# Optimization experiments

Hardware: AMD Instinct MI355X
Metric: run time of the kernel (lower is better)

## Reference

```python
import jax, jax.numpy as jnp
import numpy as np

B, T, C = 2, 4096, 768
NH = 12
HD = C // NH  # 64


def setup_inputs() -> dict:
    key = jax.random.key(0)
    k0, k1, k2, k3, k4 = jax.random.split(key, 5)
    x = jax.random.normal(k0, (B, T, C), dtype=jnp.float32)
    # parameters (stored as [in, out] for x @ W)
    w_attn = jax.random.normal(k1, (C, 3 * C), dtype=jnp.float32) * 0.02
    b_attn = jnp.zeros((3 * C,), dtype=jnp.float32)
    w_proj = jax.random.normal(k2, (C, C), dtype=jnp.float32) * 0.02
    b_proj = jnp.zeros((C,), dtype=jnp.float32)
    return {"x": x, "w_attn": w_attn, "b_attn": b_attn, "w_proj": w_proj, "b_proj": b_proj}


def reference(x, w_attn, b_attn, w_proj, b_proj):
    Bv, Tv, Cv = x.shape
    qkv = x @ w_attn + b_attn  # (B,T,3C)
    q, k, v = jnp.split(qkv, 3, axis=2)
    # (B, NH, T, HD)
    q = q.reshape(Bv, Tv, NH, HD).transpose(0, 2, 1, 3)
    k = k.reshape(Bv, Tv, NH, HD).transpose(0, 2, 1, 3)
    v = v.reshape(Bv, Tv, NH, HD).transpose(0, 2, 1, 3)
    att = jnp.einsum('bhqd,bhkd->bhqk', q, k) / jnp.sqrt(jnp.float32(HD))
    causal = jnp.tril(jnp.ones((Tv, Tv), dtype=bool))  # mask buffer slice
    att = jnp.where(causal[None, None, :, :], att, jnp.float32(-jnp.inf))
    att = jax.nn.softmax(att, axis=-1)
    y = jnp.einsum('bhqk,bhkd->bhqd', att, v)
    y = y.transpose(0, 2, 1, 3).reshape(Bv, Tv, Cv)
    y = y @ w_proj + b_proj
    return y
```

## Files before the change

### kernel.cpp

```cpp
#include <hip/hip_runtime.h>

typedef __bf16 bf16;
typedef float f32x4 __attribute__((ext_vector_type(4)));
typedef bf16 bf16x8v __attribute__((ext_vector_type(8)));
typedef bf16 bf16x4v __attribute__((ext_vector_type(4)));

#define MFMA_BF16(a, b, c) __builtin_amdgcn_mfma_f32_16x16x32_bf16((a), (b), (c), 0, 0, 0)

__device__ __forceinline__ void async16(const bf16* g, bf16* l) {
  __builtin_amdgcn_global_load_lds(
      (const __attribute__((address_space(1))) void*)g,
      (__attribute__((address_space(3))) void*)l, 16, 0, 0);
}

__global__ __launch_bounds__(256) void convert_kernel(
    const float* __restrict__ in, bf16* __restrict__ out, int n8) {
  int i = blockIdx.x * 256 + threadIdx.x;
  if (i >= n8) return;
  const float4* p = (const float4*)in + (size_t)i * 2;
  float4 a = p[0], b = p[1];
  bf16x8v o;
  o[0] = (bf16)a.x; o[1] = (bf16)a.y; o[2] = (bf16)a.z; o[3] = (bf16)a.w;
  o[4] = (bf16)b.x; o[5] = (bf16)b.y; o[6] = (bf16)b.z; o[7] = (bf16)b.w;
  ((bf16x8v*)out)[i] = o;
}

__global__ __launch_bounds__(256) void transpose_conv_kernel(
    const float* __restrict__ in, bf16* __restrict__ out, int R, int Ccols) {
  __shared__ float tile[32][33];
  int c0 = blockIdx.x * 32, r0 = blockIdx.y * 32;
  int tx = threadIdx.x & 31;
  int ty = threadIdx.x >> 5;
#pragma unroll
  for (int i = 0; i < 4; ++i) {
    int r = ty + i * 8;
    tile[r][tx] = in[(size_t)(r0 + r) * Ccols + c0 + tx];
  }
  __syncthreads();
#pragma unroll
  for (int i = 0; i < 4; ++i) {
    int c = ty + i * 8;
    out[(size_t)(c0 + c) * R + r0 + tx] = (bf16)tile[tx][c];
  }
}

__global__ __launch_bounds__(256) void transpose_bf16_kernel(
    const bf16* __restrict__ in, bf16* __restrict__ out, int R, int Ccols) {
  __shared__ bf16 tile[32][33];
  const bf16* inp = in + (size_t)blockIdx.z * R * Ccols;
  bf16* outp = out + (size_t)blockIdx.z * R * Ccols;
  int c0 = blockIdx.x * 32, r0 = blockIdx.y * 32;
  int tx = threadIdx.x & 31;
  int ty = threadIdx.x >> 5;
#pragma unroll
  for (int i = 0; i < 4; ++i) {
    int r = ty + i * 8;
    tile[r][tx] = inp[(size_t)(r0 + r) * Ccols + c0 + tx];
  }
  __syncthreads();
#pragma unroll
  for (int i = 0; i < 4; ++i) {
    int c = ty + i * 8;
    outp[(size_t)(c0 + c) * R + r0 + tx] = tile[tx][c];
  }
}

template <int MODE>
__global__ __launch_bounds__(256) void gemm_kernel(
    const bf16* __restrict__ A, const bf16* __restrict__ Bt,
    const float* __restrict__ bias, int N, float* __restrict__ outf,
    bf16* __restrict__ qo, bf16* __restrict__ ko, bf16* __restrict__ vo) {
  constexpr int Kdim = 768;
  __shared__ __align__(16) bf16 As[128][32];
  __shared__ __align__(16) bf16 Bs[128][32];
  const int tid = threadIdx.x;
  const int lane = tid & 63;
  const int wave = tid >> 6;
  const int wm = (wave >> 1) * 64, wn = (wave & 1) * 64;
  const int m0 = blockIdx.y * 128, n0 = blockIdx.x * 128;
  const int l15 = lane & 15, q4 = lane >> 4;

  f32x4 acc[4][4] = {};

  const int ca = wave * 2;
  const int ar = lane >> 2;
  const int ac = (lane & 3) * 8;
  bf16* asBase = &As[0][0];
  bf16* bsBase = &Bs[0][0];

  for (int k0 = 0; k0 < Kdim; k0 += 32) {
    const bf16* gA = A + (size_t)(m0 + ca * 16 + ar) * Kdim + k0 + ac;
    async16(gA, asBase + ca * 512);
    async16(gA + 16 * Kdim, asBase + (ca + 1) * 512);
    const bf16* gB = Bt + (size_t)(n0 + ca * 16 + ar) * Kdim + k0 + ac;
    async16(gB, bsBase + ca * 512);
    async16(gB + 16 * Kdim, bsBase + (ca + 1) * 512);
    __syncthreads();
    bf16x8v af[4], bfg[4];
#pragma unroll
    for (int i = 0; i < 4; ++i)
      af[i] = *(const bf16x8v*)&As[wm + i * 16 + l15][q4 * 8];
#pragma unroll
    for (int i = 0; i < 4; ++i)
      bfg[i] = *(const bf16x8v*)&Bs[wn + i * 16 + l15][q4 * 8];
#pragma unroll
    for (int mi = 0; mi < 4; ++mi)
#pragma unroll
      for (int ni = 0; ni < 4; ++ni)
        acc[mi][ni] = MFMA_BF16(af[mi], bfg[ni], acc[mi][ni]);
    __syncthreads();
  }

#pragma unroll
  for (int mi = 0; mi < 4; ++mi) {
#pragma unroll
    for (int ni = 0; ni < 4; ++ni) {
      int col = n0 + wn + ni * 16 + l15;
      float bv = bias[col];
#pragma unroll
      for (int r = 0; r < 4; ++r) {
        int row = m0 + wm + mi * 16 + q4 * 4 + r;
        float val = acc[mi][ni][r] + bv;
        if (MODE == 0) {
          outf[(size_t)row * N + col] = val;
        } else {
          int sel = col / 768;
          int cc = col - sel * 768;
          int h = cc >> 6, d = cc & 63;
          int b = row >> 12, t = row & 4095;
          bf16* dst = sel == 0 ? qo : (sel == 1 ? ko : vo);
          dst[((size_t)(b * 12 + h) * 4096 + t) * 64 + d] = (bf16)val;
        }
      }
    }
  }
}

__global__ __launch_bounds__(256, 3) void attn_kernel(
    const bf16* __restrict__ q, const bf16* __restrict__ k,
    const bf16* __restrict__ vt, bf16* __restrict__ y) {
  __shared__ __align__(16) bf16 Kb[2][64][64];
  __shared__ __align__(16) bf16 Vb[2][64][64];
  __shared__ __align__(16) bf16 Ps[4][32][64];
  const int tid = threadIdx.x;
  const int lane = tid & 63, wave = tid >> 6;
  const int l15 = lane & 15, q4 = lane >> 4;
  const int swz = l15 & 7;
  const int id = blockIdx.x;
  const int bh = id % 24;
  const int p = id / 24;
  const int rs0 = (63 - p) * 64 + wave * 16;
  const int rs1 = p * 64 + wave * 16;
  const int hb = bh % 12, bb = bh / 12;

  const int gr = lane >> 3;
  const int sj = (lane & 7) ^ gr;
  const bf16* kgbase = k + (size_t)bh * 4096 * 64;
  const bf16* vgbase = vt + (size_t)bh * 64 * 4096;

  bf16x8v ones;
#pragma unroll
  for (int j = 0; j < 8; ++j) ones[j] = (bf16)1.0f;

  bf16x8v qf[2][2];
#pragma unroll
  for (int st = 0; st < 2; ++st) {
    const int rs = st ? rs1 : rs0;
    const bf16* qrow = q + ((size_t)bh * 4096 + rs + l15) * 64 + q4 * 8;
#pragma unroll
    for (int ks = 0; ks < 2; ++ks) {
      bf16x8v t8 = *(const bf16x8v*)(qrow + ks * 32);
#pragma unroll
      for (int j = 0; j < 8; ++j) t8[j] = (bf16)((float)t8[j] * 0.18033688f);
      qf[st][ks] = t8;
    }
  }

  f32x4 o0[4] = {}, o1[4] = {};
  f32x4 ol0 = {}, ol1 = {};

  auto stage = [&](int kt, int buf) {
    const int t0k = kt * 64;
#pragma unroll
    for (int g = 0; g < 2; ++g) {
      const int grp = wave * 2 + g;
      async16(kgbase + (size_t)(t0k + grp * 8 + gr) * 64 + sj * 8,
              &Kb[buf][grp * 8][0]);
      async16(vgbase + (size_t)(grp * 8 + gr) * 4096 + t0k + sj * 8,
              &Vb[buf][grp * 8][0]);
    }
  };

  auto sm_full = [&](f32x4 (&s)[4]) {
#pragma unroll
    for (int ni = 0; ni < 4; ++ni)
#pragma unroll
      for (int r = 0; r < 4; ++r)
        s[ni][r] = __builtin_amdgcn_exp2f(s[ni][r] - 28.8539008f);
  };
  auto sm_mask = [&](f32x4 (&s)[4], int lim) {
#pragma unroll
    for (int ni = 0; ni < 4; ++ni)
#pragma unroll
      for (int r = 0; r < 4; ++r)
        s[ni][r] = (ni * 16 + q4 * 4 + r <= lim)
                       ? __builtin_amdgcn_exp2f(s[ni][r] - 28.8539008f)
                       : 0.0f;
  };
  auto pwrite = [&](const f32x4 (&s)[4], int row) {
#pragma unroll
    for (int ni = 0; ni < 4; ++ni) {
      bf16x4v pv4;
#pragma unroll
      for (int e = 0; e < 4; ++e) pv4[e] = (bf16)s[ni][e];
      const int jb = ni * 2 + (q4 >> 1);
      *(bf16x4v*)&Ps[wave][row][((jb ^ (row & 7)) * 8) + (q4 & 1) * 4] = pv4;
    }
  };

  const int ktmax = 64 - p;
  stage(0, 0);

  for (int kt = 0; kt < ktmax; ++kt) {
    const int buf = kt & 1;
    __syncthreads();
    if (kt + 1 < ktmax) stage(kt + 1, buf ^ 1);
    const int t0 = kt * 64;
    const bool act1 = (t0 <= rs1 + 15);

    f32x4 s0[4] = {}, s1[4] = {};
    __builtin_amdgcn_s_setprio(1);
    if (act1) {
#pragma unroll
      for (int ni = 0; ni < 4; ++ni) {
#pragma unroll
        for (int ks = 0; ks < 2; ++ks) {
          bf16x8v kf = *(const bf16x8v*)&Kb[buf][ni * 16 + l15]
                                           [((ks * 4 + q4) ^ swz) * 8];
          s0[ni] = MFMA_BF16(kf, qf[0][ks], s0[ni]);
          s1[ni] = MFMA_BF16(kf, qf[1][ks], s1[ni]);
        }
      }
    } else {
#pragma unroll
      for (int ni = 0; ni < 4; ++ni) {
#pragma unroll
        for (int ks = 0; ks < 2; ++ks) {
          bf16x8v kf = *(const bf16x8v*)&Kb[buf][ni * 16 + l15]
                                           [((ks * 4 + q4) ^ swz) * 8];
          s0[ni] = MFMA_BF16(kf, qf[0][ks], s0[ni]);
        }
      }
    }
    __builtin_amdgcn_s_setprio(0);

    if (t0 + 63 <= rs0) sm_full(s0); else sm_mask(s0, rs0 + l15 - t0);
    pwrite(s0, l15);
    if (act1) {
      if (t0 + 63 <= rs1) sm_full(s1); else sm_mask(s1, rs1 + l15 - t0);
      pwrite(s1, 16 + l15);
    }

    bf16x8v pf0[2], pf1[2];
#pragma unroll
    for (int ks = 0; ks < 2; ++ks)
      pf0[ks] = *(const bf16x8v*)&Ps[wave][l15][((ks * 4 + q4) ^ swz) * 8];
    if (act1) {
#pragma unroll
      for (int ks = 0; ks < 2; ++ks)
        pf1[ks] =
            *(const bf16x8v*)&Ps[wave][16 + l15][((ks * 4 + q4) ^ swz) * 8];
      __builtin_amdgcn_s_setprio(1);
#pragma unroll
      for (int d4 = 0; d4 < 4; ++d4) {
#pragma unroll
        for (int ks = 0; ks < 2; ++ks) {
          bf16x8v vf = *(const bf16x8v*)&Vb[buf][d4 * 16 + l15]
                                           [((ks * 4 + q4) ^ swz) * 8];
          o0[d4] = MFMA_BF16(pf0[ks], vf, o0[d4]);
          o1[d4] = MFMA_BF16(pf1[ks], vf, o1[d4]);
        }
      }
#pragma unroll
      for (int ks = 0; ks < 2; ++ks) {
        ol0 = MFMA_BF16(pf0[ks], ones, ol0);
        ol1 = MFMA_BF16(pf1[ks], ones, ol1);
      }
      __builtin_amdgcn_s_setprio(0);
    } else {
      __builtin_amdgcn_s_setprio(1);
#pragma unroll
      for (int d4 = 0; d4 < 4; ++d4) {
#pragma unroll
        for (int ks = 0; ks < 2; ++ks) {
          bf16x8v vf = *(const bf16x8v*)&Vb[buf][d4 * 16 + l15]
                                           [((ks * 4 + q4) ^ swz) * 8];
          o0[d4] = MFMA_BF16(pf0[ks], vf, o0[d4]);
        }
      }
#pragma unroll
      for (int ks = 0; ks < 2; ++ks) ol0 = MFMA_BF16(pf0[ks], ones, ol0);
      __builtin_amdgcn_s_setprio(0);
    }
  }

#pragma unroll
  for (int d4 = 0; d4 < 4; ++d4)
#pragma unroll
    for (int r = 0; r < 4; ++r) {
      int row0 = rs0 + q4 * 4 + r;
      y[((size_t)(bb * 4096 + row0)) * 768 + hb * 64 + d4 * 16 + l15] =
          (bf16)(o0[d4][r] / ol0[r]);
      int row1 = rs1 + q4 * 4 + r;
      y[((size_t)(bb * 4096 + row1)) * 768 + hb * 64 + d4 * 16 + l15] =
          (bf16)(o1[d4][r] / ol1[r]);
    }
}

extern "C" void kernel_launch(void* const* d_in, const int* in_sizes, int n_in,
                              void* d_out, int out_size, void* d_ws,
                              size_t ws_size, hipStream_t stream) {
  const float* x = (const float*)d_in[0];
  const float* w_attn = (const float*)d_in[1];
  const float* b_attn = (const float*)d_in[2];
  const float* w_proj = (const float*)d_in[3];
  const float* b_proj = (const float*)d_in[4];
  float* out = (float*)d_out;

  char* ws = (char*)d_ws;
  size_t off = 0;
  auto carve = [&](size_t elems) {
    char* p = ws + off;
    off += ((elems * sizeof(bf16) + 255) & ~(size_t)255);
    return (bf16*)p;
  };
  bf16* xb = carve((size_t)8192 * 768);
  bf16* wt_attn = carve((size_t)2304 * 768);
  bf16* wt_proj = carve((size_t)768 * 768);
  bf16* qb = carve((size_t)24 * 4096 * 64);
  bf16* kb = carve((size_t)24 * 4096 * 64);
  bf16* vb = carve((size_t)24 * 4096 * 64);
  bf16* vtb = xb;
  bf16* yb = vb;

  convert_kernel<<<(8192 * 768 / 8 + 255) / 256, 256, 0, stream>>>(
      x, xb, 8192 * 768 / 8);
  transpose_conv_kernel<<<dim3(2304 / 32, 768 / 32), 256, 0, stream>>>(
      w_attn, wt_attn, 768, 2304);
  transpose_conv_kernel<<<dim3(768 / 32, 768 / 32), 256, 0, stream>>>(
      w_proj, wt_proj, 768, 768);
  gemm_kernel<1><<<dim3(2304 / 128, 8192 / 128), 256, 0, stream>>>(
      xb, wt_attn, b_attn, 2304, nullptr, qb, kb, vb);
  transpose_bf16_kernel<<<dim3(64 / 32, 4096 / 32, 24), 256, 0, stream>>>(
      vb, vtb, 4096, 64);
  attn_kernel<<<dim3(768), 256, 0, stream>>>(qb, kb, vtb, yb);
  gemm_kernel<0><<<dim3(768 / 128, 8192 / 128), 256, 0, stream>>>(
      yb, wt_proj, b_proj, 768, out, nullptr, nullptr, nullptr);
}
```

Baseline: 240.6 us.

## Transpose MFMA operands for vectorized GEMM epilogue stores and remap attention blocks

The GEMM swaps MFMA A/B operands so each lane holds four consecutive columns of one row. This lets the epilogue do float4 bias loads and float4 or bf16x4 stores instead of scattered scalar writes. Separately, the attention kernel's block-to-(head, pair) mapping is permuted so that concurrently resident blocks cover different causal row pairs. The aim is better L2 locality and load balance. The new attention index mapping assumes a 768-block grid layout and must stay a bijection.

```diff
diff --git a/kernel.cpp b/kernel.cpp
--- a/kernel.cpp
+++ b/kernel.cpp
@@ -107,30 +107,32 @@
     for (int mi = 0; mi < 4; ++mi)
 #pragma unroll
       for (int ni = 0; ni < 4; ++ni)
-        acc[mi][ni] = MFMA_BF16(af[mi], bfg[ni], acc[mi][ni]);
+        acc[mi][ni] = MFMA_BF16(bfg[ni], af[mi], acc[mi][ni]);
     __syncthreads();
   }
 
 #pragma unroll
   for (int mi = 0; mi < 4; ++mi) {
+    const int row = m0 + wm + mi * 16 + l15;
 #pragma unroll
     for (int ni = 0; ni < 4; ++ni) {
-      int col = n0 + wn + ni * 16 + l15;
-      float bv = bias[col];
-#pragma unroll
-      for (int r = 0; r < 4; ++r) {
-        int row = m0 + wm + mi * 16 + q4 * 4 + r;
-        float val = acc[mi][ni][r] + bv;
-        if (MODE == 0) {
-          outf[(size_t)row * N + col] = val;
-        } else {
-          int sel = col / 768;
-          int cc = col - sel * 768;
-          int h = cc >> 6, d = cc & 63;
-          int b = row >> 12, t = row & 4095;
-          bf16* dst = sel == 0 ? qo : (sel == 1 ? ko : vo);
-          dst[((size_t)(b * 12 + h) * 4096 + t) * 64 + d] = (bf16)val;
-        }
+      const int colb = n0 + wn + ni * 16 + q4 * 4;
+      float4 bv = *(const float4*)&bias[colb];
+      f32x4 v = acc[mi][ni];
+      v[0] += bv.x; v[1] += bv.y; v[2] += bv.z; v[3] += bv.w;
+      if (MODE == 0) {
+        *(float4*)&outf[(size_t)row * N + colb] =
+            make_float4(v[0], v[1], v[2], v[3]);
+      } else {
+        int sel = colb / 768;
+        int cc = colb - sel * 768;
+        int h = cc >> 6, d = cc & 63;
+        int b = row >> 12, t = row & 4095;
+        bf16* dst = sel == 0 ? qo : (sel == 1 ? ko : vo);
+        bf16x4v o4;
+        o4[0] = (bf16)v[0]; o4[1] = (bf16)v[1];
+        o4[2] = (bf16)v[2]; o4[3] = (bf16)v[3];
+        *(bf16x4v*)&dst[((size_t)(b * 12 + h) * 4096 + t) * 64 + d] = o4;
       }
     }
   }
@@ -147,8 +149,12 @@
   const int l15 = lane & 15, q4 = lane >> 4;
   const int swz = l15 & 7;
   const int id = blockIdx.x;
-  const int bh = id % 24;
-  const int p = id / 24;
+  const int uu = id & 255, rr = id >> 8;
+  const int gg = uu >> 5, ii = uu & 31;
+  const int bh = gg * 3 + rr;
+  const int p = (rr == 0) ? ii
+              : (rr == 1) ? ((ii < 16) ? 30 - 2 * ii : 63 - 2 * ii)
+                          : ((ii + 16) & 31);
   const int rs0 = (63 - p) * 64 + wave * 16;
   const int rs1 = p * 64 + wave * 16;
   const int hb = bh % 12, bb = bh / 12;
```

Result: slower. 271.1 us (+12.7%).

## Split attention query strips across eight waves instead of two per wave

Applied to the files above, without the earlier changes.

The attention block grows from 256 to 512 threads. Each wave now owns one 16-row query strip: waves 0-3 take the late causal strip and waves 4-7 the early one. Before, each wave computed both strips, sharing K fragment loads between them. This lowers register pressure per wave and raises wave-level parallelism, and waves whose strip is fully masked idle at barriers instead of branching. The cost is losing K/V fragment reuse across the two strips, so each LDS fragment is read twice, and the early-strip waves sit idle at barriers for much of the loop.

```diff
diff --git a/kernel.cpp b/kernel.cpp
--- a/kernel.cpp
+++ b/kernel.cpp
@@ -136,12 +136,12 @@
   }
 }
 
-__global__ __launch_bounds__(256, 3) void attn_kernel(
+__global__ __launch_bounds__(512, 6) void attn_kernel(
     const bf16* __restrict__ q, const bf16* __restrict__ k,
     const bf16* __restrict__ vt, bf16* __restrict__ y) {
   __shared__ __align__(16) bf16 Kb[2][64][64];
   __shared__ __align__(16) bf16 Vb[2][64][64];
-  __shared__ __align__(16) bf16 Ps[4][32][64];
+  __shared__ __align__(16) bf16 Ps[8][16][64];
   const int tid = threadIdx.x;
   const int lane = tid & 63, wave = tid >> 6;
   const int l15 = lane & 15, q4 = lane >> 4;
@@ -149,8 +149,8 @@
   const int id = blockIdx.x;
   const int bh = id % 24;
   const int p = id / 24;
-  const int rs0 = (63 - p) * 64 + wave * 16;
-  const int rs1 = p * 64 + wave * 16;
+  const int rs = (wave < 4) ? ((63 - p) * 64 + wave * 16)
+                            : (p * 64 + (wave - 4) * 16);
   const int hb = bh % 12, bb = bh / 12;
 
   const int gr = lane >> 3;
@@ -162,33 +162,27 @@
 #pragma unroll
   for (int j = 0; j < 8; ++j) ones[j] = (bf16)1.0f;
 
-  bf16x8v qf[2][2];
-#pragma unroll
-  for (int st = 0; st < 2; ++st) {
-    const int rs = st ? rs1 : rs0;
+  bf16x8v qf[2];
+  {
     const bf16* qrow = q + ((size_t)bh * 4096 + rs + l15) * 64 + q4 * 8;
 #pragma unroll
     for (int ks = 0; ks < 2; ++ks) {
       bf16x8v t8 = *(const bf16x8v*)(qrow + ks * 32);
 #pragma unroll
       for (int j = 0; j < 8; ++j) t8[j] = (bf16)((float)t8[j] * 0.18033688f);
-      qf[st][ks] = t8;
-    }
-  }
-
-  f32x4 o0[4] = {}, o1[4] = {};
-  f32x4 ol0 = {}, ol1 = {};
+      qf[ks] = t8;
+    }
+  }
+
+  f32x4 o[4] = {};
+  f32x4 ol = {};
 
   auto stage = [&](int kt, int buf) {
     const int t0k = kt * 64;
-#pragma unroll
-    for (int g = 0; g < 2; ++g) {
-      const int grp = wave * 2 + g;
-      async16(kgbase + (size_t)(t0k + grp * 8 + gr) * 64 + sj * 8,
-              &Kb[buf][grp * 8][0]);
-      async16(vgbase + (size_t)(grp * 8 + gr) * 4096 + t0k + sj * 8,
-              &Vb[buf][grp * 8][0]);
-    }
+    async16(kgbase + (size_t)(t0k + wave * 8 + gr) * 64 + sj * 8,
+            &Kb[buf][wave * 8][0]);
+    async16(vgbase + (size_t)(wave * 8 + gr) * 4096 + t0k + sj * 8,
+            &Vb[buf][wave * 8][0]);
   };
 
   auto sm_full = [&](f32x4 (&s)[4]) {
@@ -207,14 +201,14 @@
                        ? __builtin_amdgcn_exp2f(s[ni][r] - 28.8539008f)
                        : 0.0f;
   };
-  auto pwrite = [&](const f32x4 (&s)[4], int row) {
+  auto pwrite = [&](const f32x4 (&s)[4]) {
 #pragma unroll
     for (int ni = 0; ni < 4; ++ni) {
       bf16x4v pv4;
 #pragma unroll
       for (int e = 0; e < 4; ++e) pv4[e] = (bf16)s[ni][e];
       const int jb = ni * 2 + (q4 >> 1);
-      *(bf16x4v*)&Ps[wave][row][((jb ^ (row & 7)) * 8) + (q4 & 1) * 4] = pv4;
+      *(bf16x4v*)&Ps[wave][l15][((jb ^ (l15 & 7)) * 8) + (q4 & 1) * 4] = pv4;
     }
   };
 
@@ -226,50 +220,29 @@
     __syncthreads();
     if (kt + 1 < ktmax) stage(kt + 1, buf ^ 1);
     const int t0 = kt * 64;
-    const bool act1 = (t0 <= rs1 + 15);
-
-    f32x4 s0[4] = {}, s1[4] = {};
-    __builtin_amdgcn_s_setprio(1);
-    if (act1) {
+
+    if (t0 <= rs + 15) {
+      f32x4 s[4] = {};
+      __builtin_amdgcn_s_setprio(1);
 #pragma unroll
       for (int ni = 0; ni < 4; ++ni) {
 #pragma unroll
         for (int ks = 0; ks < 2; ++ks) {
           bf16x8v kf = *(const bf16x8v*)&Kb[buf][ni * 16 + l15]
                                            [((ks * 4 + q4) ^ swz) * 8];
-          s0[ni] = MFMA_BF16(kf, qf[0][ks], s0[ni]);
-          s1[ni] = MFMA_BF16(kf, qf[1][ks], s1[ni]);
+          s[ni] = MFMA_BF16(kf, qf[ks], s[ni]);
         }
       }
-    } else {
-#pragma unroll
-      for (int ni = 0; ni < 4; ++ni) {
-#pragma unroll
-        for (int ks = 0; ks < 2; ++ks) {
-          bf16x8v kf = *(const bf16x8v*)&Kb[buf][ni * 16 + l15]
-                                           [((ks * 4 + q4) ^ swz) * 8];
-          s0[ni] = MFMA_BF16(kf, qf[0][ks], s0[ni]);
-        }
-      }
-    }
-    __builtin_amdgcn_s_setprio(0);
-
-    if (t0 + 63 <= rs0) sm_full(s0); else sm_mask(s0, rs0 + l15 - t0);
-    pwrite(s0, l15);
-    if (act1) {
-      if (t0 + 63 <= rs1) sm_full(s1); else sm_mask(s1, rs1 + l15 - t0);
-      pwrite(s1, 16 + l15);
-    }
-
-    bf16x8v pf0[2], pf1[2];
-#pragma unroll
-    for (int ks = 0; ks < 2; ++ks)
-      pf0[ks] = *(const bf16x8v*)&Ps[wave][l15][((ks * 4 + q4) ^ swz) * 8];
-    if (act1) {
+      __builtin_amdgcn_s_setprio(0);
+
+      if (t0 + 63 <= rs) sm_full(s); else sm_mask(s, rs + l15 - t0);
+      pwrite(s);
+
+      bf16x8v pf[2];
 #pragma unroll
       for (int ks = 0; ks < 2; ++ks)
-        pf1[ks] =
-            *(const bf16x8v*)&Ps[wave][16 + l15][((ks * 4 + q4) ^ swz) * 8];
+        pf[ks] = *(const bf16x8v*)&Ps[wave][l15][((ks * 4 + q4) ^ swz) * 8];
+
       __builtin_amdgcn_s_setprio(1);
 #pragma unroll
       for (int d4 = 0; d4 < 4; ++d4) {
@@ -277,30 +250,12 @@
         for (int ks = 0; ks < 2; ++ks) {
           bf16x8v vf = *(const bf16x8v*)&Vb[buf][d4 * 16 + l15]
                                            [((ks * 4 + q4) ^ swz) * 8];
-          o0[d4] = MFMA_BF16(pf0[ks], vf, o0[d4]);
-          o1[d4] = MFMA_BF16(pf1[ks], vf, o1[d4]);
+          o[d4] = MFMA_BF16(pf[ks], vf, o[d4]);
         }
       }
 #pragma unroll
-      for (int ks = 0; ks < 2; ++ks) {
-        ol0 = MFMA_BF16(pf0[ks], ones, ol0);
-        ol1 = MFMA_BF16(pf1[ks], ones, ol1);
-      }
+      for (int ks = 0; ks < 2; ++ks) ol = MFMA_BF16(pf[ks], ones, ol);
       __builtin_amdgcn_s_setprio(0);
-    } else {
-      __builtin_amdgcn_s_setprio(1);
-#pragma unroll
-      for (int d4 = 0; d4 < 4; ++d4) {
-#pragma unroll
-        for (int ks = 0; ks < 2; ++ks) {
-          bf16x8v vf = *(const bf16x8v*)&Vb[buf][d4 * 16 + l15]
-                                           [((ks * 4 + q4) ^ swz) * 8];
-          o0[d4] = MFMA_BF16(pf0[ks], vf, o0[d4]);
-        }
-      }
-#pragma unroll
-      for (int ks = 0; ks < 2; ++ks) ol0 = MFMA_BF16(pf0[ks], ones, ol0);
-      __builtin_amdgcn_s_setprio(0);
     }
   }
 
@@ -308,12 +263,9 @@
   for (int d4 = 0; d4 < 4; ++d4)
 #pragma unroll
     for (int r = 0; r < 4; ++r) {
-      int row0 = rs0 + q4 * 4 + r;
-      y[((size_t)(bb * 4096 + row0)) * 768 + hb * 64 + d4 * 16 + l15] =
-          (bf16)(o0[d4][r] / ol0[r]);
-      int row1 = rs1 + q4 * 4 + r;
-      y[((size_t)(bb * 4096 + row1)) * 768 + hb * 64 + d4 * 16 + l15] =
-          (bf16)(o1[d4][r] / ol1[r]);
+      int row = rs + q4 * 4 + r;
+      y[((size_t)(bb * 4096 + row)) * 768 + hb * 64 + d4 * 16 + l15] =
+          (bf16)(o[d4][r] / ol[r]);
     }
 }
 
@@ -353,7 +305,7 @@
       xb, wt_attn, b_attn, 2304, nullptr, qb, kb, vb);
   transpose_bf16_kernel<<<dim3(64 / 32, 4096 / 32, 24), 256, 0, stream>>>(
       vb, vtb, 4096, 64);
-  attn_kernel<<<dim3(768), 256, 0, stream>>>(qb, kb, vtb, yb);
+  attn_kernel<<<dim3(768), 512, 0, stream>>>(qb, kb, vtb, yb);
   gemm_kernel<0><<<dim3(768 / 128, 8192 / 128), 256, 0, stream>>>(
       yb, wt_proj, b_proj, 768, out, nullptr, nullptr, nullptr);
 }
```

Result: no change. 242.1 us (+0.6%).
